# Kernel optimization log

Measured on AMD Instinct MI355X. Metric: run time of the kernel, lower is better.

The kernel has to match this reference:

```python
import jax, jax.numpy as jnp
import numpy as np

N_NODES = 170000
N_EDGES = 1200000
F_IN, HID, N_CLS = 128, 64, 40
N_CONVS = 7  # num_layers - 1
ALPHA, THETA = 0.1, 0.5


def setup_inputs() -> dict:
    key = jax.random.key(0)
    ks = jax.random.split(key, 8)
    x = jax.random.normal(ks[0], (N_NODES, F_IN), dtype=jnp.float32)
    edge_src = jax.random.randint(ks[1], (N_EDGES,), 0, N_NODES, dtype=jnp.int32)
    edge_dst = jax.random.randint(ks[2], (N_EDGES,), 0, N_NODES, dtype=jnp.int32)
    # pre-normalized adjacency values (normalize=False in GCN2Conv)
    edge_weight = jax.random.uniform(ks[3], (N_EDGES,), dtype=jnp.float32)
    W_in = jax.random.normal(ks[4], (F_IN, HID), dtype=jnp.float32) / np.sqrt(F_IN)
    b_in = jnp.zeros((HID,), dtype=jnp.float32)
    conv_W = jax.random.normal(ks[5], (N_CONVS, HID, HID), dtype=jnp.float32) / np.sqrt(HID)
    W_out = jax.random.normal(ks[6], (HID, N_CLS), dtype=jnp.float32) / np.sqrt(HID)
    b_out = jnp.zeros((N_CLS,), dtype=jnp.float32)
    return {"x": x, "edge_src": edge_src, "edge_dst": edge_dst,
            "edge_weight": edge_weight, "W_in": W_in, "b_in": b_in,
            "conv_W": conv_W, "W_out": W_out, "b_out": b_out}


def reference(x, edge_src, edge_dst, edge_weight, W_in, b_in, conv_W, W_out, b_out):
    n = x.shape[0]
    h = jax.nn.relu(x @ W_in + b_in)          # [N, HID]
    x0 = h                                    # initial residual
    for l in range(conv_W.shape[0]):
        beta = float(np.log(THETA / (l + 1) + 1.0))
        # SpMM: adj_t @ h  (gather from source, weighted scatter-add to target)
        msg = h[edge_src] * edge_weight[:, None]             # [E, HID]
        agg = jax.ops.segment_sum(msg, edge_dst, num_segments=n)
        hh = (1.0 - ALPHA) * agg + ALPHA * x0                # initial residual mix
        h = jax.nn.relu((1.0 - beta) * hh + beta * (hh @ conv_W[l]))  # identity mapping
    out = h @ W_out + b_out
    return jax.nn.log_softmax(out, axis=-1)
```

## Files before the change

kernel.cpp:

```cpp
#include <hip/hip_runtime.h>
#include <math.h>

typedef _Float16 f16x8 __attribute__((ext_vector_type(8)));
typedef float f32x4 __attribute__((ext_vector_type(4)));

__device__ __forceinline__ float us2f(unsigned short u) {
  _Float16 h;
  __builtin_memcpy(&h, &u, 2);
  return (float)h;
}
__device__ __forceinline__ unsigned short f2us(float f) {
  _Float16 h = (_Float16)f;
  unsigned short u;
  __builtin_memcpy(&u, &h, 2);
  return u;
}

__global__ __launch_bounds__(256) void hist_k(const int* __restrict__ dst, int* __restrict__ deg,
                                              int E, int N) {
  int xcd = blockIdx.x & 7;
  int bid = blockIdx.x >> 3;
  int nb = gridDim.x >> 3;
  int R = (N + 7) >> 3;
  int lo = xcd * R;
  int hi = min(N, lo + R);
  for (int e = bid * blockDim.x + threadIdx.x; e < E; e += nb * blockDim.x) {
    int d = dst[e];
    if (d >= lo && d < hi) atomicAdd(&deg[d], 1);
  }
}

__global__ __launch_bounds__(1024) void scan1_k(const int* __restrict__ deg, int* __restrict__ rp,
                                                int* __restrict__ bsum, int n) {
  __shared__ int buf[2][1024];
  int tid = threadIdx.x;
  int i = blockIdx.x * 1024 + tid;
  int v = (i < n) ? deg[i] : 0;
  int pp = 0;
  buf[0][tid] = v;
  __syncthreads();
  for (int off = 1; off < 1024; off <<= 1) {
    int t = buf[pp][tid];
    if (tid >= off) t += buf[pp][tid - off];
    buf[pp ^ 1][tid] = t;
    pp ^= 1;
    __syncthreads();
  }
  int inc = buf[pp][tid];
  if (i < n) rp[i] = inc - v;
  if (tid == 1023) bsum[blockIdx.x] = inc;
}

__global__ __launch_bounds__(256) void scan2_k(int* __restrict__ bsum, int nb) {
  __shared__ int buf[2][256];
  int tid = threadIdx.x;
  int v = (tid < nb) ? bsum[tid] : 0;
  int pp = 0;
  buf[0][tid] = v;
  __syncthreads();
  for (int off = 1; off < 256; off <<= 1) {
    int t = buf[pp][tid];
    if (tid >= off) t += buf[pp][tid - off];
    buf[pp ^ 1][tid] = t;
    pp ^= 1;
    __syncthreads();
  }
  if (tid < nb) bsum[tid] = buf[pp][tid] - v;
}

__global__ __launch_bounds__(1024) void scan3_k(int* __restrict__ rp, int* __restrict__ cur,
                                                const int* __restrict__ bsum, int n, int E) {
  int i = blockIdx.x * 1024 + threadIdx.x;
  if (i < n) {
    int v = rp[i] + bsum[blockIdx.x];
    rp[i] = v;
    cur[i] = v;
  }
  if (i == 0) rp[n] = E;
}

__global__ __launch_bounds__(256) void scatter_k(const int* __restrict__ src, const int* __restrict__ dst,
                                                 const float* __restrict__ w, int* __restrict__ cur,
                                                 int2* __restrict__ edge, int E, int N) {
  int xcd = blockIdx.x & 7;
  int bid = blockIdx.x >> 3;
  int nb = gridDim.x >> 3;
  int R = (N + 7) >> 3;
  int lo = xcd * R;
  int hi = min(N, lo + R);
  for (int e = bid * blockDim.x + threadIdx.x; e < E; e += nb * blockDim.x) {
    int d = dst[e];
    if (d >= lo && d < hi) {
      int pos = atomicAdd(&cur[d], 1);
      edge[pos] = make_int2(src[e], __float_as_int(w[e]));
    }
  }
}

__global__ __launch_bounds__(256) void ingemm_k(const float* __restrict__ x, const float* __restrict__ Win,
                                                const float* __restrict__ bin, unsigned short* __restrict__ x0,
                                                int n) {
  int lane = threadIdx.x & 63;
  int wave = threadIdx.x >> 6;
  int col = lane & 15, grp = lane >> 4;
  f16x8 B[4][4];
#pragma unroll
  for (int c = 0; c < 4; ++c)
#pragma unroll
    for (int t = 0; t < 4; ++t) {
      f16x8 b;
#pragma unroll
      for (int j = 0; j < 8; ++j) b[j] = (_Float16)Win[(c * 32 + grp * 8 + j) * 64 + t * 16 + col];
      B[c][t] = b;
    }
  float bb[4];
#pragma unroll
  for (int t = 0; t < 4; ++t) bb[t] = bin[t * 16 + col];

  int node_base = (blockIdx.x * 4 + wave) * 16;
  if (node_base >= n) return;
  int arow = node_base + col;
  if (arow > n - 1) arow = n - 1;
  const float* xr = x + (size_t)arow * 128 + grp * 8;

  f32x4 acc[4];
  f32x4 z = {0.f, 0.f, 0.f, 0.f};
#pragma unroll
  for (int t = 0; t < 4; ++t) acc[t] = z;
#pragma unroll
  for (int c = 0; c < 4; ++c) {
    f32x4 lo = *(const f32x4*)(xr + c * 32);
    f32x4 hi = *(const f32x4*)(xr + c * 32 + 4);
    f16x8 a;
#pragma unroll
    for (int j = 0; j < 4; ++j) a[j] = (_Float16)lo[j];
#pragma unroll
    for (int j = 0; j < 4; ++j) a[4 + j] = (_Float16)hi[j];
#pragma unroll
    for (int t = 0; t < 4; ++t) acc[t] = __builtin_amdgcn_mfma_f32_16x16x32_f16(a, B[c][t], acc[t], 0, 0, 0);
  }
#pragma unroll
  for (int t = 0; t < 4; ++t)
#pragma unroll
    for (int r = 0; r < 4; ++r) {
      int node = node_base + grp * 4 + r;
      if (node < n) {
        float o = acc[t][r] + bb[t];
        x0[(size_t)node * 64 + t * 16 + col] = f2us(fmaxf(o, 0.f));
      }
    }
}

__global__ __launch_bounds__(256) void spmm_k(const ushort4* __restrict__ hin4,
                                              const ushort4* __restrict__ x04,
                                              const int* __restrict__ rp, const int2* __restrict__ edge,
                                              ushort4* __restrict__ hh4, int n) {
  int lane = threadIdx.x & 63;
  int wave = threadIdx.x >> 6;
  int q = lane >> 4;
  int sl = lane & 15;
  int S = gridDim.x * 16;
  for (int node = (blockIdx.x * 4 + wave) * 4 + q; node < n; node += S) {
    int beg = rp[node], end = rp[node + 1];
    ushort4 xv = x04[(size_t)node * 16 + sl];
    float a0 = 0.f, a1 = 0.f, a2 = 0.f, a3 = 0.f;
    for (int e = beg; e < end; e += 8) {
      int2 d[8];
#pragma unroll
      for (int j = 0; j < 8; ++j) d[j] = (e + j < end) ? edge[e + j] : make_int2(0, 0);
      ushort4 v[8];
#pragma unroll
      for (int j = 0; j < 8; ++j) v[j] = hin4[(size_t)d[j].x * 16 + sl];
#pragma unroll
      for (int j = 0; j < 8; ++j) {
        float w = __int_as_float(d[j].y);
        a0 = fmaf(us2f(v[j].x), w, a0);
        a1 = fmaf(us2f(v[j].y), w, a1);
        a2 = fmaf(us2f(v[j].z), w, a2);
        a3 = fmaf(us2f(v[j].w), w, a3);
      }
    }
    ushort4 o;
    o.x = f2us(fmaf(0.9f, a0, 0.1f * us2f(xv.x)));
    o.y = f2us(fmaf(0.9f, a1, 0.1f * us2f(xv.y)));
    o.z = f2us(fmaf(0.9f, a2, 0.1f * us2f(xv.z)));
    o.w = f2us(fmaf(0.9f, a3, 0.1f * us2f(xv.w)));
    hh4[(size_t)node * 16 + sl] = o;
  }
}

__global__ __launch_bounds__(256) void gemm_k(const unsigned short* __restrict__ hh,
                                              const float* __restrict__ W, unsigned short* __restrict__ hout,
                                              float beta, int n) {
  int lane = threadIdx.x & 63;
  int wave = threadIdx.x >> 6;
  int col = lane & 15, grp = lane >> 4;
  f16x8 B[2][4];
#pragma unroll
  for (int c = 0; c < 2; ++c)
#pragma unroll
    for (int t = 0; t < 4; ++t) {
      f16x8 b;
#pragma unroll
      for (int j = 0; j < 8; ++j) b[j] = (_Float16)W[(c * 32 + grp * 8 + j) * 64 + t * 16 + col];
      B[c][t] = b;
    }
  int node_base = (blockIdx.x * 4 + wave) * 16;
  if (node_base >= n) return;
  int arow = node_base + col;
  if (arow > n - 1) arow = n - 1;
  const unsigned short* rowp = hh + (size_t)arow * 64 + grp * 8;
  f16x8 A0 = *(const f16x8*)(rowp);
  f16x8 A1 = *(const f16x8*)(rowp + 32);

  f32x4 acc[4];
  f32x4 z = {0.f, 0.f, 0.f, 0.f};
#pragma unroll
  for (int t = 0; t < 4; ++t) acc[t] = z;
#pragma unroll
  for (int t = 0; t < 4; ++t) {
    acc[t] = __builtin_amdgcn_mfma_f32_16x16x32_f16(A0, B[0][t], acc[t], 0, 0, 0);
    acc[t] = __builtin_amdgcn_mfma_f32_16x16x32_f16(A1, B[1][t], acc[t], 0, 0, 0);
  }
  float ob = 1.f - beta;
#pragma unroll
  for (int t = 0; t < 4; ++t)
#pragma unroll
    for (int r = 0; r < 4; ++r) {
      int node = node_base + grp * 4 + r;
      if (node < n) {
        float hv = us2f(hh[(size_t)node * 64 + t * 16 + col]);
        float o = ob * hv + beta * acc[t][r];
        hout[(size_t)node * 64 + t * 16 + col] = f2us(fmaxf(o, 0.f));
      }
    }
}

__global__ __launch_bounds__(256) void out_k(const unsigned short* __restrict__ h,
                                             const float* __restrict__ Wout, const float* __restrict__ bout,
                                             float* __restrict__ out, int n) {
  int lane = threadIdx.x & 63;
  int wave = threadIdx.x >> 6;
  int col = lane & 15, grp = lane >> 4;
  f16x8 B[2][3];
#pragma unroll
  for (int c = 0; c < 2; ++c)
#pragma unroll
    for (int t = 0; t < 3; ++t) {
      int cls = t * 16 + col;
      f16x8 b;
#pragma unroll
      for (int j = 0; j < 8; ++j) b[j] = (cls < 40) ? (_Float16)Wout[(c * 32 + grp * 8 + j) * 40 + cls] : (_Float16)0.f;
      B[c][t] = b;
    }
  float bb[3];
#pragma unroll
  for (int t = 0; t < 3; ++t) {
    int cls = t * 16 + col;
    bb[t] = (cls < 40) ? bout[cls] : 0.f;
  }
  int node_base = (blockIdx.x * 4 + wave) * 16;
  if (node_base >= n) return;
  int arow = node_base + col;
  if (arow > n - 1) arow = n - 1;
  const unsigned short* rowp = h + (size_t)arow * 64 + grp * 8;
  f16x8 A0 = *(const f16x8*)(rowp);
  f16x8 A1 = *(const f16x8*)(rowp + 32);

  f32x4 acc[3];
  f32x4 z = {0.f, 0.f, 0.f, 0.f};
#pragma unroll
  for (int t = 0; t < 3; ++t) acc[t] = z;
#pragma unroll
  for (int t = 0; t < 3; ++t) {
    acc[t] = __builtin_amdgcn_mfma_f32_16x16x32_f16(A0, B[0][t], acc[t], 0, 0, 0);
    acc[t] = __builtin_amdgcn_mfma_f32_16x16x32_f16(A1, B[1][t], acc[t], 0, 0, 0);
  }
#pragma unroll
  for (int r = 0; r < 4; ++r) {
    int node = node_base + grp * 4 + r;
    float v0 = acc[0][r] + bb[0];
    float v1 = acc[1][r] + bb[1];
    float v2 = (32 + col < 40) ? (acc[2][r] + bb[2]) : -INFINITY;
    float m = fmaxf(fmaxf(v0, v1), v2);
#pragma unroll
    for (int mask = 1; mask <= 8; mask <<= 1) m = fmaxf(m, __shfl_xor(m, mask, 64));
    float p = expf(v0 - m) + expf(v1 - m) + ((32 + col < 40) ? expf(v2 - m) : 0.f);
#pragma unroll
    for (int mask = 1; mask <= 8; mask <<= 1) p += __shfl_xor(p, mask, 64);
    float ml = m + logf(p);
    if (node < n) {
      out[(size_t)node * 40 + col] = v0 - ml;
      out[(size_t)node * 40 + 16 + col] = v1 - ml;
      if (32 + col < 40) out[(size_t)node * 40 + 32 + col] = v2 - ml;
    }
  }
}

extern "C" void kernel_launch(void* const* d_in, const int* in_sizes, int n_in,
                              void* d_out, int out_size, void* d_ws, size_t ws_size,
                              hipStream_t stream) {
  const float* x = (const float*)d_in[0];
  const int* esrc = (const int*)d_in[1];
  const int* edst = (const int*)d_in[2];
  const float* ew = (const float*)d_in[3];
  const float* Win = (const float*)d_in[4];
  const float* bin = (const float*)d_in[5];
  const float* convW = (const float*)d_in[6];
  const float* Wout = (const float*)d_in[7];
  const float* bout = (const float*)d_in[8];
  float* out = (float*)d_out;

  const int N = in_sizes[0] / 128;
  const int E = in_sizes[1];
  const int NC = in_sizes[6] / (64 * 64);

  char* ws = (char*)d_ws;
  size_t off = 0;
  auto alloc = [&](size_t b) {
    void* p = ws + off;
    off += (b + 255) & ~(size_t)255;
    return p;
  };
  unsigned short* x0 = (unsigned short*)alloc((size_t)N * 64 * 2);
  unsigned short* ha = (unsigned short*)alloc((size_t)N * 64 * 2);
  unsigned short* hb = (unsigned short*)alloc((size_t)N * 64 * 2);
  unsigned short* hhb = (unsigned short*)alloc((size_t)N * 64 * 2);
  int* deg = (int*)alloc((size_t)N * 4);
  int* rp = (int*)alloc((size_t)(N + 1) * 4);
  int* cur = (int*)alloc((size_t)N * 4);
  int* bsum = (int*)alloc(1024);
  int2* edge = (int2*)alloc((size_t)E * 8);

  hipMemsetAsync(deg, 0, (size_t)N * 4, stream);
  hist_k<<<2048, 256, 0, stream>>>(edst, deg, E, N);
  int nb = (N + 1023) / 1024;
  scan1_k<<<nb, 1024, 0, stream>>>(deg, rp, bsum, N);
  scan2_k<<<1, 256, 0, stream>>>(bsum, nb);
  scan3_k<<<nb, 1024, 0, stream>>>(rp, cur, bsum, N, E);
  scatter_k<<<2048, 256, 0, stream>>>(esrc, edst, ew, cur, edge, E, N);

  int gblocks = (N + 63) / 64;
  ingemm_k<<<gblocks, 256, 0, stream>>>(x, Win, bin, x0, N);

  const unsigned short* hin = x0;
  unsigned short* bufs[2] = {ha, hb};
  for (int l = 0; l < NC; ++l) {
    float beta = logf(0.5f / (float)(l + 1) + 1.0f);
    unsigned short* ho = bufs[l & 1];
    spmm_k<<<2048, 256, 0, stream>>>((const ushort4*)hin, (const ushort4*)x0, rp, edge, (ushort4*)hhb, N);
    gemm_k<<<gblocks, 256, 0, stream>>>(hhb, convW + (size_t)l * 64 * 64, ho, beta, N);
    hin = ho;
  }
  out_k<<<gblocks, 256, 0, stream>>>(hin, Wout, bout, out, N);
}
```

Before: 561.7 us.

## Fuse SpMM with layer GEMM, add split-f16 MFMA, edge sort, nontemporal loads

Merges the per-layer SpMM and dense GEMM into one kernel that keeps the aggregated rows in shared memory, removing the hh round trip through global memory and one launch per layer. It also adds a per-node selection sort of each CSR row by original edge index, which makes summation order deterministic, and splits every GEMM into hi/lo f16 parts for near-fp32 accuracy. Loads and stores are marked nontemporal. The split GEMMs roughly triple MFMA work, and the serial per-node sort adds setup cost.

```diff
diff --git a/kernel.cpp b/kernel.cpp
--- a/kernel.cpp
+++ b/kernel.cpp
@@ -14,6 +14,18 @@
   unsigned short u;
   __builtin_memcpy(&u, &h, 2);
   return u;
+}
+__device__ __forceinline__ int2 nt_load_i2(const int2* p) {
+  long long raw = __builtin_nontemporal_load((const long long*)p);
+  int2 v;
+  __builtin_memcpy(&v, &raw, 8);
+  return v;
+}
+__device__ __forceinline__ ushort4 nt_load_us4(const ushort4* p) {
+  unsigned long long raw = __builtin_nontemporal_load((const unsigned long long*)p);
+  ushort4 v;
+  __builtin_memcpy(&v, &raw, 8);
+  return v;
 }
 
 __global__ __launch_bounds__(256) void hist_k(const int* __restrict__ dst, int* __restrict__ deg,
@@ -25,7 +37,7 @@
   int lo = xcd * R;
   int hi = min(N, lo + R);
   for (int e = bid * blockDim.x + threadIdx.x; e < E; e += nb * blockDim.x) {
-    int d = dst[e];
+    int d = __builtin_nontemporal_load(dst + e);
     if (d >= lo && d < hi) atomicAdd(&deg[d], 1);
   }
 }
@@ -81,7 +93,8 @@
 
 __global__ __launch_bounds__(256) void scatter_k(const int* __restrict__ src, const int* __restrict__ dst,
                                                  const float* __restrict__ w, int* __restrict__ cur,
-                                                 int2* __restrict__ edge, int E, int N) {
+                                                 int2* __restrict__ edge, int* __restrict__ eidx,
+                                                 int E, int N) {
   int xcd = blockIdx.x & 7;
   int bid = blockIdx.x >> 3;
   int nb = gridDim.x >> 3;
@@ -89,10 +102,34 @@
   int lo = xcd * R;
   int hi = min(N, lo + R);
   for (int e = bid * blockDim.x + threadIdx.x; e < E; e += nb * blockDim.x) {
-    int d = dst[e];
+    int d = __builtin_nontemporal_load(dst + e);
+    int s = __builtin_nontemporal_load(src + e);
+    float ww = __builtin_nontemporal_load(w + e);
     if (d >= lo && d < hi) {
       int pos = atomicAdd(&cur[d], 1);
-      edge[pos] = make_int2(src[e], __float_as_int(w[e]));
+      edge[pos] = make_int2(s, __float_as_int(ww));
+      eidx[pos] = e;
+    }
+  }
+}
+
+__global__ __launch_bounds__(256) void sortpack_k(int* __restrict__ eidx, int2* __restrict__ edge,
+                                                  const int* __restrict__ rp, int n) {
+  int node = blockIdx.x * 256 + threadIdx.x;
+  if (node >= n) return;
+  int beg = rp[node], end = rp[node + 1];
+  for (int i = beg; i < end - 1; ++i) {
+    int mi = i, mv = eidx[i];
+    for (int j = i + 1; j < end; ++j) {
+      int v = eidx[j];
+      if (v < mv) { mv = v; mi = j; }
+    }
+    if (mi != i) {
+      eidx[mi] = eidx[i];
+      eidx[i] = mv;
+      int2 t = edge[i];
+      edge[i] = edge[mi];
+      edge[mi] = t;
     }
   }
 }
@@ -103,15 +140,21 @@
   int lane = threadIdx.x & 63;
   int wave = threadIdx.x >> 6;
   int col = lane & 15, grp = lane >> 4;
-  f16x8 B[4][4];
+  f16x8 Bh[4][4], Bl[4][4];
 #pragma unroll
   for (int c = 0; c < 4; ++c)
 #pragma unroll
     for (int t = 0; t < 4; ++t) {
-      f16x8 b;
-#pragma unroll
-      for (int j = 0; j < 8; ++j) b[j] = (_Float16)Win[(c * 32 + grp * 8 + j) * 64 + t * 16 + col];
-      B[c][t] = b;
+      f16x8 bh, bl;
+#pragma unroll
+      for (int j = 0; j < 8; ++j) {
+        float wv = Win[(c * 32 + grp * 8 + j) * 64 + t * 16 + col];
+        _Float16 hi = (_Float16)wv;
+        bh[j] = hi;
+        bl[j] = (_Float16)(wv - (float)hi);
+      }
+      Bh[c][t] = bh;
+      Bl[c][t] = bl;
     }
   float bb[4];
 #pragma unroll
@@ -131,13 +174,22 @@
   for (int c = 0; c < 4; ++c) {
     f32x4 lo = *(const f32x4*)(xr + c * 32);
     f32x4 hi = *(const f32x4*)(xr + c * 32 + 4);
-    f16x8 a;
-#pragma unroll
-    for (int j = 0; j < 4; ++j) a[j] = (_Float16)lo[j];
-#pragma unroll
-    for (int j = 0; j < 4; ++j) a[4 + j] = (_Float16)hi[j];
-#pragma unroll
-    for (int t = 0; t < 4; ++t) acc[t] = __builtin_amdgcn_mfma_f32_16x16x32_f16(a, B[c][t], acc[t], 0, 0, 0);
+    f16x8 ah, al;
+#pragma unroll
+    for (int j = 0; j < 4; ++j) {
+      _Float16 h0 = (_Float16)lo[j];
+      ah[j] = h0;
+      al[j] = (_Float16)(lo[j] - (float)h0);
+      _Float16 h1 = (_Float16)hi[j];
+      ah[4 + j] = h1;
+      al[4 + j] = (_Float16)(hi[j] - (float)h1);
+    }
+#pragma unroll
+    for (int t = 0; t < 4; ++t) {
+      acc[t] = __builtin_amdgcn_mfma_f32_16x16x32_f16(ah, Bh[c][t], acc[t], 0, 0, 0);
+      acc[t] = __builtin_amdgcn_mfma_f32_16x16x32_f16(al, Bh[c][t], acc[t], 0, 0, 0);
+      acc[t] = __builtin_amdgcn_mfma_f32_16x16x32_f16(ah, Bl[c][t], acc[t], 0, 0, 0);
+    }
   }
 #pragma unroll
   for (int t = 0; t < 4; ++t)
@@ -151,67 +203,78 @@
     }
 }
 
-__global__ __launch_bounds__(256) void spmm_k(const ushort4* __restrict__ hin4,
-                                              const ushort4* __restrict__ x04,
-                                              const int* __restrict__ rp, const int2* __restrict__ edge,
-                                              ushort4* __restrict__ hh4, int n) {
+__global__ __launch_bounds__(256) void layer_fused_k(const ushort4* __restrict__ hin4,
+                                                     const ushort4* __restrict__ x04,
+                                                     const int* __restrict__ rp, const int2* __restrict__ edge,
+                                                     const float* __restrict__ W,
+                                                     unsigned short* __restrict__ hout,
+                                                     float beta, int n) {
+  __shared__ float hh_lds[64][72];
   int lane = threadIdx.x & 63;
   int wave = threadIdx.x >> 6;
   int q = lane >> 4;
   int sl = lane & 15;
-  int S = gridDim.x * 16;
-  for (int node = (blockIdx.x * 4 + wave) * 4 + q; node < n; node += S) {
-    int beg = rp[node], end = rp[node + 1];
-    ushort4 xv = x04[(size_t)node * 16 + sl];
+  int blockStart = blockIdx.x * 64;
+
+#pragma unroll
+  for (int r = 0; r < 4; ++r) {
+    int nib = wave * 16 + r * 4 + q;
+    int node = blockStart + nib;
     float a0 = 0.f, a1 = 0.f, a2 = 0.f, a3 = 0.f;
-    for (int e = beg; e < end; e += 8) {
-      int2 d[8];
-#pragma unroll
-      for (int j = 0; j < 8; ++j) d[j] = (e + j < end) ? edge[e + j] : make_int2(0, 0);
-      ushort4 v[8];
-#pragma unroll
-      for (int j = 0; j < 8; ++j) v[j] = hin4[(size_t)d[j].x * 16 + sl];
+    ushort4 xv = make_ushort4(0, 0, 0, 0);
+    if (node < n) {
+      int beg = __builtin_nontemporal_load(rp + node);
+      int end = __builtin_nontemporal_load(rp + node + 1);
+      xv = nt_load_us4(x04 + (size_t)node * 16 + sl);
+      for (int e = beg; e < end; e += 8) {
+        int2 d[8];
+#pragma unroll
+        for (int j = 0; j < 8; ++j) d[j] = (e + j < end) ? nt_load_i2(edge + e + j) : make_int2(0, 0);
+        ushort4 v[8];
+#pragma unroll
+        for (int j = 0; j < 8; ++j) v[j] = hin4[(size_t)d[j].x * 16 + sl];
+#pragma unroll
+        for (int j = 0; j < 8; ++j) {
+          float w = __int_as_float(d[j].y);
+          a0 = fmaf(us2f(v[j].x), w, a0);
+          a1 = fmaf(us2f(v[j].y), w, a1);
+          a2 = fmaf(us2f(v[j].z), w, a2);
+          a3 = fmaf(us2f(v[j].w), w, a3);
+        }
+      }
+    }
+    float4 o;
+    o.x = fmaf(0.9f, a0, 0.1f * us2f(xv.x));
+    o.y = fmaf(0.9f, a1, 0.1f * us2f(xv.y));
+    o.z = fmaf(0.9f, a2, 0.1f * us2f(xv.z));
+    o.w = fmaf(0.9f, a3, 0.1f * us2f(xv.w));
+    *(float4*)&hh_lds[nib][sl * 4] = o;
+  }
+  __syncthreads();
+
+  int col = lane & 15, grp = lane >> 4;
+  f16x8 Bh[2][4], Bl[2][4];
+#pragma unroll
+  for (int c = 0; c < 2; ++c)
+#pragma unroll
+    for (int t = 0; t < 4; ++t) {
+      f16x8 bh, bl;
 #pragma unroll
       for (int j = 0; j < 8; ++j) {
-        float w = __int_as_float(d[j].y);
-        a0 = fmaf(us2f(v[j].x), w, a0);
-        a1 = fmaf(us2f(v[j].y), w, a1);
-        a2 = fmaf(us2f(v[j].z), w, a2);
-        a3 = fmaf(us2f(v[j].w), w, a3);
-      }
-    }
-    ushort4 o;
-    o.x = f2us(fmaf(0.9f, a0, 0.1f * us2f(xv.x)));
-    o.y = f2us(fmaf(0.9f, a1, 0.1f * us2f(xv.y)));
-    o.z = f2us(fmaf(0.9f, a2, 0.1f * us2f(xv.z)));
-    o.w = f2us(fmaf(0.9f, a3, 0.1f * us2f(xv.w)));
-    hh4[(size_t)node * 16 + sl] = o;
-  }
-}
-
-__global__ __launch_bounds__(256) void gemm_k(const unsigned short* __restrict__ hh,
-                                              const float* __restrict__ W, unsigned short* __restrict__ hout,
-                                              float beta, int n) {
-  int lane = threadIdx.x & 63;
-  int wave = threadIdx.x >> 6;
-  int col = lane & 15, grp = lane >> 4;
-  f16x8 B[2][4];
-#pragma unroll
-  for (int c = 0; c < 2; ++c)
-#pragma unroll
-    for (int t = 0; t < 4; ++t) {
-      f16x8 b;
-#pragma unroll
-      for (int j = 0; j < 8; ++j) b[j] = (_Float16)W[(c * 32 + grp * 8 + j) * 64 + t * 16 + col];
-      B[c][t] = b;
-    }
-  int node_base = (blockIdx.x * 4 + wave) * 16;
-  if (node_base >= n) return;
-  int arow = node_base + col;
-  if (arow > n - 1) arow = n - 1;
-  const unsigned short* rowp = hh + (size_t)arow * 64 + grp * 8;
-  f16x8 A0 = *(const f16x8*)(rowp);
-  f16x8 A1 = *(const f16x8*)(rowp + 32);
+        float wv = W[(c * 32 + grp * 8 + j) * 64 + t * 16 + col];
+        _Float16 hi = (_Float16)wv;
+        bh[j] = hi;
+        bl[j] = (_Float16)(wv - (float)hi);
+      }
+      Bh[c][t] = bh;
+      Bl[c][t] = bl;
+    }
+  f16x8 A0, A1;
+#pragma unroll
+  for (int j = 0; j < 8; ++j) {
+    A0[j] = (_Float16)hh_lds[wave * 16 + col][j + grp * 8];
+    A1[j] = (_Float16)hh_lds[wave * 16 + col][32 + j + grp * 8];
+  }
 
   f32x4 acc[4];
   f32x4 z = {0.f, 0.f, 0.f, 0.f};
@@ -219,19 +282,22 @@
   for (int t = 0; t < 4; ++t) acc[t] = z;
 #pragma unroll
   for (int t = 0; t < 4; ++t) {
-    acc[t] = __builtin_amdgcn_mfma_f32_16x16x32_f16(A0, B[0][t], acc[t], 0, 0, 0);
-    acc[t] = __builtin_amdgcn_mfma_f32_16x16x32_f16(A1, B[1][t], acc[t], 0, 0, 0);
+    acc[t] = __builtin_amdgcn_mfma_f32_16x16x32_f16(A0, Bh[0][t], acc[t], 0, 0, 0);
+    acc[t] = __builtin_amdgcn_mfma_f32_16x16x32_f16(A1, Bh[1][t], acc[t], 0, 0, 0);
+    acc[t] = __builtin_amdgcn_mfma_f32_16x16x32_f16(A0, Bl[0][t], acc[t], 0, 0, 0);
+    acc[t] = __builtin_amdgcn_mfma_f32_16x16x32_f16(A1, Bl[1][t], acc[t], 0, 0, 0);
   }
   float ob = 1.f - beta;
+  int node_base = blockStart + wave * 16;
 #pragma unroll
   for (int t = 0; t < 4; ++t)
 #pragma unroll
     for (int r = 0; r < 4; ++r) {
       int node = node_base + grp * 4 + r;
       if (node < n) {
-        float hv = us2f(hh[(size_t)node * 64 + t * 16 + col]);
+        float hv = hh_lds[wave * 16 + grp * 4 + r][t * 16 + col];
         float o = ob * hv + beta * acc[t][r];
-        hout[(size_t)node * 64 + t * 16 + col] = f2us(fmaxf(o, 0.f));
+        __builtin_nontemporal_store(f2us(fmaxf(o, 0.f)), hout + (size_t)node * 64 + t * 16 + col);
       }
     }
 }
@@ -242,16 +308,22 @@
   int lane = threadIdx.x & 63;
   int wave = threadIdx.x >> 6;
   int col = lane & 15, grp = lane >> 4;
-  f16x8 B[2][3];
+  f16x8 Bh[2][3], Bl[2][3];
 #pragma unroll
   for (int c = 0; c < 2; ++c)
 #pragma unroll
     for (int t = 0; t < 3; ++t) {
       int cls = t * 16 + col;
-      f16x8 b;
-#pragma unroll
-      for (int j = 0; j < 8; ++j) b[j] = (cls < 40) ? (_Float16)Wout[(c * 32 + grp * 8 + j) * 40 + cls] : (_Float16)0.f;
-      B[c][t] = b;
+      f16x8 bh, bl;
+#pragma unroll
+      for (int j = 0; j < 8; ++j) {
+        float wv = (cls < 40) ? Wout[(c * 32 + grp * 8 + j) * 40 + cls] : 0.f;
+        _Float16 hi = (_Float16)wv;
+        bh[j] = hi;
+        bl[j] = (_Float16)(wv - (float)hi);
+      }
+      Bh[c][t] = bh;
+      Bl[c][t] = bl;
     }
   float bb[3];
 #pragma unroll
@@ -273,8 +345,10 @@
   for (int t = 0; t < 3; ++t) acc[t] = z;
 #pragma unroll
   for (int t = 0; t < 3; ++t) {
-    acc[t] = __builtin_amdgcn_mfma_f32_16x16x32_f16(A0, B[0][t], acc[t], 0, 0, 0);
-    acc[t] = __builtin_amdgcn_mfma_f32_16x16x32_f16(A1, B[1][t], acc[t], 0, 0, 0);
+    acc[t] = __builtin_amdgcn_mfma_f32_16x16x32_f16(A0, Bh[0][t], acc[t], 0, 0, 0);
+    acc[t] = __builtin_amdgcn_mfma_f32_16x16x32_f16(A1, Bh[1][t], acc[t], 0, 0, 0);
+    acc[t] = __builtin_amdgcn_mfma_f32_16x16x32_f16(A0, Bl[0][t], acc[t], 0, 0, 0);
+    acc[t] = __builtin_amdgcn_mfma_f32_16x16x32_f16(A1, Bl[1][t], acc[t], 0, 0, 0);
   }
 #pragma unroll
   for (int r = 0; r < 4; ++r) {
@@ -325,12 +399,12 @@
   unsigned short* x0 = (unsigned short*)alloc((size_t)N * 64 * 2);
   unsigned short* ha = (unsigned short*)alloc((size_t)N * 64 * 2);
   unsigned short* hb = (unsigned short*)alloc((size_t)N * 64 * 2);
-  unsigned short* hhb = (unsigned short*)alloc((size_t)N * 64 * 2);
   int* deg = (int*)alloc((size_t)N * 4);
   int* rp = (int*)alloc((size_t)(N + 1) * 4);
   int* cur = (int*)alloc((size_t)N * 4);
   int* bsum = (int*)alloc(1024);
   int2* edge = (int2*)alloc((size_t)E * 8);
+  int* eidx = (int*)alloc((size_t)E * 4);
 
   hipMemsetAsync(deg, 0, (size_t)N * 4, stream);
   hist_k<<<2048, 256, 0, stream>>>(edst, deg, E, N);
@@ -338,7 +412,8 @@
   scan1_k<<<nb, 1024, 0, stream>>>(deg, rp, bsum, N);
   scan2_k<<<1, 256, 0, stream>>>(bsum, nb);
   scan3_k<<<nb, 1024, 0, stream>>>(rp, cur, bsum, N, E);
-  scatter_k<<<2048, 256, 0, stream>>>(esrc, edst, ew, cur, edge, E, N);
+  scatter_k<<<2048, 256, 0, stream>>>(esrc, edst, ew, cur, edge, eidx, E, N);
+  sortpack_k<<<(N + 255) / 256, 256, 0, stream>>>(eidx, edge, rp, N);
 
   int gblocks = (N + 63) / 64;
   ingemm_k<<<gblocks, 256, 0, stream>>>(x, Win, bin, x0, N);
@@ -348,8 +423,8 @@
   for (int l = 0; l < NC; ++l) {
     float beta = logf(0.5f / (float)(l + 1) + 1.0f);
     unsigned short* ho = bufs[l & 1];
-    spmm_k<<<2048, 256, 0, stream>>>((const ushort4*)hin, (const ushort4*)x0, rp, edge, (ushort4*)hhb, N);
-    gemm_k<<<gblocks, 256, 0, stream>>>(hhb, convW + (size_t)l * 64 * 64, ho, beta, N);
+    layer_fused_k<<<gblocks, 256, 0, stream>>>((const ushort4*)hin, (const ushort4*)x0, rp, edge,
+                                               convW + (size_t)l * 64 * 64, ho, beta, N);
     hin = ho;
   }
   out_k<<<gblocks, 256, 0, stream>>>(hin, Wout, bout, out, N);
```

New measurement: 863.7 us. +53.8%, slower.
